# Kernel optimization log

Hardware: AMD Instinct MI355X
Metric: run time of the kernel (lower is better)

## Reference

```python
import jax, jax.numpy as jnp
import numpy as np
from jax import lax

# pywt 'db6' rec_lo (scaling filter). dec_lo = rec_lo[::-1]; pytorch_wavelets
# stores dec filters flipped for conv (=correlation), so analysis correlation
# filters are exactly rec_lo and rec_hi = qmf(rec_lo). Synthesis filters for
# conv_transpose are rec_lo/rec_hi unflipped -> same arrays.
_DB6 = np.array([0.11154074335008017, 0.4946238903983854, 0.7511339080215775,
                 0.3152503517092432, -0.22626469396516913, -0.12976686756709563,
                 0.09750160558707936, 0.02752286553001629, -0.031582039318031156,
                 0.0005538422009938016, 0.004777257511010651, -0.00107730108499558],
                dtype=np.float32)
_QMF = (_DB6[::-1].copy() * ((-1.0) ** np.arange(12))).astype(np.float32)
H0, H1 = jnp.asarray(_DB6), jnp.asarray(_QMF)
LF, J = 12, 3
BATCH, SEQ_LEN, CH = 128, 720, 321
COMP_L = [99, 365, 188, 99]   # [yl, yh1, yh2, yh3] for seq_len=720
OUT_L = [22, 57, 34, 22]      # same decomposition of red_len=104


def afb1d(x):
    """One-level analysis filter bank, mode='symmetric'. x: [B,C,N]."""
    B, C, N = x.shape
    out = (N + LF - 1) // 2                      # pywt dwt_coeff_len (symmetric)
    p = 2 * (out - 1) - N + LF
    xp = jnp.pad(x, ((0, 0), (0, 0), (p // 2, (p + 1) // 2)), mode='symmetric')
    w = jnp.stack([H0, H1])[:, None, :]          # [2,1,LF]
    y = lax.conv_general_dilated(xp.reshape(B * C, 1, -1), w, (2,), 'VALID',
                                 dimension_numbers=('NCH', 'OIH', 'NCH'))
    y = y.reshape(B, C, 2, out)
    return y[:, :, 0], y[:, :, 1]


def sfb1d(lo, hi):
    """One-level synthesis bank == conv_transpose1d(stride=2, padding=LF-2)."""
    B, C, Lin = lo.shape
    z = jnp.stack([lo, hi], axis=2).reshape(B * C, 2, Lin)
    w = jnp.stack([H0[::-1], H1[::-1]])[None]    # [1,2,LF], flipped for corr
    y = lax.conv_general_dilated(z, w, (1,), ((1, 1),), lhs_dilation=(2,),
                                 dimension_numbers=('NCH', 'OIH', 'NCH'))
    return y.reshape(B, C, -1)                   # length 2*Lin + 2 - LF


def sinusoidal_pe(n_pos, d):
    pos = jnp.arange(n_pos, dtype=jnp.float32)[:, None]
    div = jnp.exp(jnp.arange(0, d, 2, dtype=jnp.float32) * (-np.log(10000.0) / d))
    pe = jnp.zeros((n_pos, d), jnp.float32)
    pe = pe.at[:, 0::2].set(jnp.sin(pos * div))
    pe = pe.at[:, 1::2].set(jnp.cos(pos * div[: d // 2]))
    return pe


def _forward(x, qws, qbs, kws, kbs, pws, pbs, iws, als, bes):
    mean = lax.stop_gradient(jnp.mean(x, axis=1, keepdims=True))
    std = lax.stop_gradient(jnp.sqrt(jnp.var(x, axis=1, keepdims=True) + 1e-5))
    xc = jnp.transpose((x - mean) / std, (0, 2, 1))      # [B,C,L]
    yl, yh = xc, []
    for _ in range(J):
        yl, hi = afb1d(yl)
        yh.append(hi)
    decomps = [yl] + yh                                  # lengths COMP_L
    preds = []
    for i, comp in enumerate(decomps):
        B, C, L = comp.shape
        Q = jnp.tanh(comp @ qws[i].T + qbs[i])           # [B,C,L]
        K = jnp.tanh(comp @ kws[i].T + kbs[i])
        scores = jnp.einsum('bcl,bcs->bls', Q, K) / (L ** 0.5)
        weighted = jnp.mean(jnp.tanh(scores), axis=1)    # [B,S] (equal per channel)
        cum = jnp.flip(jnp.cumsum(jnp.flip(weighted, -1), -1), -1)
        P = jax.nn.softmax(cum * als[i][0], axis=-1)
        idxs = jnp.arange(L, dtype=jnp.float32)
        win = jnp.sum(P * idxs, axis=-1)[:, None, None]  # soft truncation [B,1,1]
        mask = jax.nn.sigmoid((idxs[None, None, :] - win) * bes[i][0])
        pred = (comp * mask) @ pws[i].T + pbs[i]         # [B,C,O]
        pred = jax.nn.softmax(iws[i], axis=1) * (pred + sinusoidal_pe(C, pred.shape[-1])[None])
        preds.append(pred)
    ll = preds[0]
    for h in preds[:0:-1]:                               # coarsest high band first
        if ll.shape[-1] > h.shape[-1]:
            ll = ll[..., : h.shape[-1]]
        ll = sfb1d(ll, h)
    return ll, mean, std


def setup_inputs() -> dict:
    key = jax.random.key(0)
    ks = jax.random.split(key, 64)
    inp = {'x': jax.random.normal(ks[0], (BATCH, SEQ_LEN, CH), jnp.float32)}
    k = 1
    for i, (L, O) in enumerate(zip(COMP_L, OUT_L)):
        s = 1.0 / np.sqrt(L)                             # torch Linear default init
        inp[f'qw{i}'] = jax.random.uniform(ks[k], (L, L), jnp.float32, -s, s); k += 1
        inp[f'qb{i}'] = jax.random.uniform(ks[k], (L,), jnp.float32, -s, s); k += 1
        inp[f'kw{i}'] = jax.random.uniform(ks[k], (L, L), jnp.float32, -s, s); k += 1
        inp[f'kb{i}'] = jax.random.uniform(ks[k], (L,), jnp.float32, -s, s); k += 1
        inp[f'pw{i}'] = jnp.full((O, L), 1.0 / L, jnp.float32)
        inp[f'pb{i}'] = jnp.zeros((O,), jnp.float32)
        inp[f'iw{i}'] = jnp.ones((1, CH, O), jnp.float32)
        inp[f'al{i}'] = jnp.full((1,), 10.0, jnp.float32)
        inp[f'be{i}'] = jnp.full((1,), 10.0, jnp.float32)
    return inp


def reference(x, qw0, qb0, kw0, kb0, pw0, pb0, iw0, al0, be0,
              qw1, qb1, kw1, kb1, pw1, pb1, iw1, al1, be1,
              qw2, qb2, kw2, kb2, pw2, pb2, iw2, al2, be2,
              qw3, qb3, kw3, kb3, pw3, pb3, iw3, al3, be3):
    return _forward(x, [qw0, qw1, qw2, qw3], [qb0, qb1, qb2, qb3],
                    [kw0, kw1, kw2, kw3], [kb0, kb1, kb2, kb3],
                    [pw0, pw1, pw2, pw3], [pb0, pb1, pb2, pb3],
                    [iw0, iw1, iw2, iw3], [al0, al1, al2, al3],
                    [be0, be1, be2, be3])
```

## Files before the change

kernel.cpp:

```cpp
#include <hip/hip_runtime.h>
#include <hip/hip_bf16.h>
#include <math.h>

namespace {
constexpr int kB  = 128;
constexpr int kC  = 321;
constexpr int kN0 = 720;
constexpr int kCp = 384;
}

typedef __attribute__((ext_vector_type(8))) short short8;
typedef __attribute__((ext_vector_type(4))) float floatx4;

__constant__ float c_h0[12] = {
  0.11154074335008017f, 0.4946238903983854f, 0.7511339080215775f,
  0.3152503517092432f, -0.22626469396516913f, -0.12976686756709563f,
  0.09750160558707936f, 0.02752286553001629f, -0.031582039318031156f,
  0.0005538422009938016f, 0.004777257511010651f, -0.00107730108499558f};
__constant__ float c_h1[12] = {
  -0.00107730108499558f, -0.004777257511010651f, 0.0005538422009938016f,
  0.031582039318031156f, 0.02752286553001629f, -0.09750160558707936f,
  -0.12976686756709563f, 0.22626469396516913f, 0.3152503517092432f,
  -0.7511339080215775f, 0.4946238903983854f, -0.11154074335008017f};
__constant__ float c_h0r[12] = {
  -0.00107730108499558f, 0.004777257511010651f, 0.0005538422009938016f,
  -0.031582039318031156f, 0.02752286553001629f, 0.09750160558707936f,
  -0.12976686756709563f, -0.22626469396516913f, 0.3152503517092432f,
  0.7511339080215775f, 0.4946238903983854f, 0.11154074335008017f};
__constant__ float c_h1r[12] = {
  -0.11154074335008017f, 0.4946238903983854f, -0.7511339080215775f,
  0.3152503517092432f, 0.22626469396516913f, -0.12976686756709563f,
  -0.09750160558707936f, 0.02752286553001629f, 0.031582039318031156f,
  0.0005538422009938016f, -0.004777257511010651f, -0.00107730108499558f};

__device__ __forceinline__ float fast_tanh(float x) {
  float e = __expf(2.f * x);
  return 1.f - 2.f / (e + 1.f);
}
__device__ __forceinline__ unsigned short f2b(float f) {
  __hip_bfloat16 h = __float2bfloat16(f);
  return __builtin_bit_cast(unsigned short, h);
}

__device__ __forceinline__ void gload16(const unsigned short* g, short* l) {
  __builtin_amdgcn_global_load_lds(
      (const __attribute__((address_space(1))) unsigned int*)g,
      (__attribute__((address_space(3))) unsigned int*)l, 16, 0, 0);
}

__global__ void __launch_bounds__(128) partial_ms_kernel(
    const float* __restrict__ x, float* __restrict__ ps, float* __restrict__ ps2) {
  int b = blockIdx.x, chunk = blockIdx.y;
  int c = blockIdx.z * 128 + threadIdx.x;
  if (c >= kC) return;
  const float* xb = x + (size_t)b * kN0 * kC + c;
  int t0 = chunk * 90;
  float s = 0.f, s2 = 0.f;
#pragma unroll 15
  for (int i = 0; i < 90; ++i) {
    float v = xb[(size_t)(t0 + i) * kC];
    s += v; s2 += v * v;
  }
  ps [(b * 8 + chunk) * kC + c] = s;
  ps2[(b * 8 + chunk) * kC + c] = s2;
}

__global__ void __launch_bounds__(256) finalize_ms_kernel(
    const float* __restrict__ ps, const float* __restrict__ ps2,
    float* __restrict__ mout, float* __restrict__ sout,
    float* __restrict__ meanw, float* __restrict__ invw) {
  int i = blockIdx.x * 256 + threadIdx.x;
  if (i >= kB * kC) return;
  int b = i / kC, c = i - b * kC;
  float s = 0.f, s2 = 0.f;
#pragma unroll
  for (int k = 0; k < 8; ++k) { s += ps[(b * 8 + k) * kC + c]; s2 += ps2[(b * 8 + k) * kC + c]; }
  float mean = s * (1.f / (float)kN0);
  float var = s2 * (1.f / (float)kN0) - mean * mean;
  float sd = sqrtf(var + 1e-5f);
  mout[i] = mean; sout[i] = sd;
  meanw[i] = mean; invw[i] = 1.f / sd;
}

__device__ __forceinline__ int sym_reflect(int t, int N) {
  t = (t < 0) ? (-1 - t) : t;
  t = (t >= N) ? (2 * N - 1 - t) : t;
  return t;
}

template <bool NORM, bool LO_F32, bool LO_BF16>
__global__ void __launch_bounds__(256) dwt_fused_kernel(
    const float* __restrict__ in, const float* __restrict__ meanw,
    const float* __restrict__ invw, float* __restrict__ loF,
    unsigned short* __restrict__ loB, unsigned short* __restrict__ hiB,
    int N, int L, int Lp) {
  __shared__ float xs[138][64];
  __shared__ unsigned short los[64][72];
  __shared__ unsigned short his[64][72];
  const int b = blockIdx.z;
  const int n0 = blockIdx.x * 64, c0 = blockIdx.y * 64;
  const int tid = threadIdx.x;
  const int cl = tid & 63, wv = tid >> 6;
  const int c = c0 + cl;
  const int t0 = 2 * n0 - 10;
  const float* ib = in + (size_t)b * N * kC;
  float mean = 0.f, inv = 1.f;
  if (NORM && c < kC) { mean = meanw[b * kC + c]; inv = invw[b * kC + c]; }
  for (int r = wv; r < 138; r += 4) {
    int t = sym_reflect(t0 + r, N);
    float v = (c < kC) ? ib[(size_t)t * kC + c] : 0.f;
    if (NORM) v = (v - mean) * inv;
    xs[r][cl] = v;
  }
  __syncthreads();
#pragma unroll 4
  for (int k = 0; k < 16; ++k) {
    int nl = wv + 4 * k;
    int n = n0 + nl;
    float a0 = 0.f, a1 = 0.f;
    int base = 2 * nl;
#pragma unroll
    for (int j = 0; j < 12; ++j) {
      float v = xs[base + j][cl];
      a0 += v * c_h0[j]; a1 += v * c_h1[j];
    }
    bool valid = (n < L) && (c < kC);
    if (LO_F32 && valid) loF[((size_t)b * L + n) * kC + c] = a0;
    if (LO_BF16) los[cl][nl] = f2b(valid ? a0 : 0.f);
    his[cl][nl] = f2b(valid ? a1 : 0.f);
  }
  __syncthreads();
  int row = tid >> 2, part = tid & 3;
  size_t dst = ((size_t)b * kCp + c0 + row) * Lp + n0 + part * 16;
  *(uint4*)(hiB + dst)     = *(const uint4*)&his[row][part * 16];
  *(uint4*)(hiB + dst + 8) = *(const uint4*)&his[row][part * 16 + 8];
  if (LO_BF16) {
    *(uint4*)(loB + dst)     = *(const uint4*)&los[row][part * 16];
    *(uint4*)(loB + dst + 8) = *(const uint4*)&los[row][part * 16 + 8];
  }
}

struct WcArgs { const float* src[8]; unsigned short* dst[8]; int L[8]; int Lp[8]; };
__global__ void __launch_bounds__(256) wconv_all_kernel(WcArgs a) {
  int lvl = blockIdx.y;
  int Lp = a.Lp[lvl], L = a.L[lvl];
  int i = blockIdx.x * 256 + threadIdx.x;
  if (i >= Lp * Lp) return;
  int p = i / Lp, l = i - p * Lp;
  a.dst[lvl][i] = f2b((p < L && l < L) ? a.src[lvl][(size_t)p * L + l] : 0.f);
}

struct QKAllArgs {
  const unsigned short* W[8];
  const unsigned short* Xt[4];
  const float* bias[8];
  unsigned short* Y[8];
  int Lp[4], L[4], yOff[4];
};
__global__ void __launch_bounds__(512, 4) qk_all_kernel(QKAllArgs a) {
  const int y = blockIdx.y;
  const int lvl = (y >= a.yOff[1]) + (y >= a.yOff[2]) + (y >= a.yOff[3]);
  const int Lp = a.Lp[lvl], L = a.L[lvl];
  const int pBase = (y - a.yOff[lvl]) * 128;
  const unsigned short* W0 = a.W[2 * lvl]     + (size_t)pBase * Lp;
  const unsigned short* W1 = a.W[2 * lvl + 1] + (size_t)pBase * Lp;
  const int b = blockIdx.z;
  const int cBase = blockIdx.x * 64;
  const int tid = threadIdx.x;
  const int ln = tid & 63, w = tid >> 6;
  __shared__ short smem[2 * 320 * 64];
  floatx4 acc[2][4] = {};
  const unsigned short* Xb = a.Xt[lvl] + ((size_t)b * kCp + cBase) * Lp;
  const int lrow = ln >> 3;
  const int gswz = ((ln & 7) ^ lrow) << 3;
  const unsigned short* srcs[5];
#pragma unroll
  for (int i = 0; i < 5; ++i) {
    int o = w * 5 + i;
    int rr = o * 8 + lrow;
    const unsigned short* s = (o < 16) ? (W0 + (size_t)rr * Lp)
                            : (o < 32) ? (W1 + (size_t)(rr - 128) * Lp)
                                       : (Xb + (size_t)(rr - 256) * Lp);
    srcs[i] = s + gswz;
  }
  const int nt = Lp >> 6;
#pragma unroll
  for (int i = 0; i < 5; ++i) gload16(srcs[i], &smem[(w * 5 + i) * 512]);
  __syncthreads();
  for (int kt = 0; kt < nt; ++kt) {
    const int ph = (kt & 1) * 20480;
    if (kt + 1 < nt) {
      const int phn = ((kt + 1) & 1) * 20480;
      const int lc = (kt + 1) << 6;
#pragma unroll
      for (int i = 0; i < 5; ++i) gload16(srcs[i] + lc, &smem[phn + (w * 5 + i) * 512]);
    }
#pragma unroll
    for (int sub = 0; sub < 2; ++sub) {
      const int sc = (((ln >> 4) + sub * 4) ^ (ln & 7)) << 3;
      const int ar = (w * 16 + (ln & 15)) * 64 + sc;
      short8 aq = *(const short8*)&smem[ph + ar];
      short8 ak = *(const short8*)&smem[ph + 8192 + ar];
      short8 bv[4];
#pragma unroll
      for (int ni = 0; ni < 4; ++ni)
        bv[ni] = *(const short8*)&smem[ph + 16384 + (ni * 16 + (ln & 15)) * 64 + sc];
#pragma unroll
      for (int ni = 0; ni < 4; ++ni) {
        acc[0][ni] = __builtin_amdgcn_mfma_f32_16x16x32_bf16(aq, bv[ni], acc[0][ni], 0, 0, 0);
        acc[1][ni] = __builtin_amdgcn_mfma_f32_16x16x32_bf16(ak, bv[ni], acc[1][ni], 0, 0, 0);
      }
    }
    __syncthreads();
  }
#pragma unroll
  for (int s = 0; s < 2; ++s) {
    const float* bias = a.bias[2 * lvl + s];
    unsigned short* Yd = a.Y[2 * lvl + s];
#pragma unroll
    for (int r = 0; r < 4; ++r) {
      int p = pBase + w * 16 + (ln >> 4) * 4 + r;
      bool pv = (p < L);
      float bvf = pv ? bias[p] : 0.f;
#pragma unroll
      for (int ni = 0; ni < 4; ++ni) {
        int c = cBase + ni * 16 + (ln & 15);
        float v = fast_tanh(acc[s][ni][r] + bvf);
        if (s == 0) { if (!pv) v = 0.f; }
        else        { if (c >= kC) v = 0.f; }
        Yd[((size_t)b * Lp + p) * kCp + c] = f2b(v);
      }
    }
  }
}

struct ScAllArgs {
  const unsigned short* Q[4]; const unsigned short* K[4];
  float* wgt[4];
  int Lp[4], L[4], tOff[4];
  float scale[4];
};
__global__ void __launch_bounds__(512, 4) scores_all_kernel(ScAllArgs a) {
  const int t = blockIdx.x;
  const int lvl = (t >= a.tOff[1]) + (t >= a.tOff[2]) + (t >= a.tOff[3]);
  const int rel = t - a.tOff[lvl];
  const int Lp = a.Lp[lvl], L = a.L[lvl];
  const int pt = Lp >> 7;
  const int sBase = (rel % pt) * 128;
  const int lBase = (rel / pt) * 128;
  const int b = blockIdx.y;
  const int tid = threadIdx.x;
  const int ln = tid & 63, w = tid >> 6;
  const int wm = w & 3, wn = w >> 2;
  __shared__ short smem[2 * 256 * 64];
  __shared__ float red[128];
  floatx4 acc[2][4] = {};
  const unsigned short* Qp = a.Q[lvl] + ((size_t)b * Lp + lBase) * kCp;
  const unsigned short* Kp = a.K[lvl] + ((size_t)b * Lp + sBase) * kCp;
  const int lrow = ln >> 3;
  const int gswz = ((ln & 7) ^ lrow) << 3;
  const unsigned short* srcs[4];
#pragma unroll
  for (int i = 0; i < 4; ++i) {
    int o = w * 4 + i;
    int rr = o * 8 + lrow;
    srcs[i] = ((o < 16) ? (Qp + (size_t)rr * kCp)
                        : (Kp + (size_t)(rr - 128) * kCp)) + gswz;
  }
#pragma unroll
  for (int i = 0; i < 4; ++i) gload16(srcs[i], &smem[(w * 4 + i) * 512]);
  if (tid < 128) red[tid] = 0.f;
  __syncthreads();
  const int nt = kCp >> 6;
  for (int kt = 0; kt < nt; ++kt) {
    const int ph = (kt & 1) * 16384;
    if (kt + 1 < nt) {
      const int phn = ((kt + 1) & 1) * 16384;
      const int cc = (kt + 1) << 6;
#pragma unroll
      for (int i = 0; i < 4; ++i) gload16(srcs[i] + cc, &smem[phn + (w * 4 + i) * 512]);
    }
#pragma unroll
    for (int sub = 0; sub < 2; ++sub) {
      const int sc = (((ln >> 4) + sub * 4) ^ (ln & 7)) << 3;
      short8 av[2], bv[4];
#pragma unroll
      for (int mi = 0; mi < 2; ++mi)
        av[mi] = *(const short8*)&smem[ph + (wm * 32 + mi * 16 + (ln & 15)) * 64 + sc];
#pragma unroll
      for (int ni = 0; ni < 4; ++ni)
        bv[ni] = *(const short8*)&smem[ph + 8192 + (wn * 64 + ni * 16 + (ln & 15)) * 64 + sc];
#pragma unroll
      for (int mi = 0; mi < 2; ++mi)
#pragma unroll
        for (int ni = 0; ni < 4; ++ni)
          acc[mi][ni] = __builtin_amdgcn_mfma_f32_16x16x32_bf16(av[mi], bv[ni], acc[mi][ni], 0, 0, 0);
    }
    __syncthreads();
  }
  const float scale = a.scale[lvl];
#pragma unroll
  for (int ni = 0; ni < 4; ++ni) {
    float p = 0.f;
#pragma unroll
    for (int mi = 0; mi < 2; ++mi)
#pragma unroll
      for (int r = 0; r < 4; ++r) p += fast_tanh(acc[mi][ni][r] * scale);
    p += __shfl_xor(p, 16);
    p += __shfl_xor(p, 32);
    if ((ln & 48) == 0) atomicAdd(&red[wn * 64 + ni * 16 + (ln & 15)], p);
  }
  __syncthreads();
  if (tid < 128) {
    int s = sBase + tid;
    if (s < L) atomicAdd(&a.wgt[lvl][(size_t)b * L + s], red[tid]);
  }
}

struct WinArgs { const float* wgt[4]; const float* al[4]; const float* be[4];
                 float* mask[4]; int L[4]; };
__global__ void __launch_bounds__(64) winmask_all_kernel(WinArgs a) {
  int lvl = blockIdx.y;
  int b = blockIdx.x, lane = threadIdx.x;
  int L = a.L[lvl];
  const float* wgt = a.wgt[lvl] + (size_t)b * L;
  float al = a.al[lvl][0], be = a.be[lvl][0];
  float invL = 1.f / (float)L;
  int chunk = (L + 63) >> 6;
  int s0 = lane * chunk;
  float v[6];
  float csum = 0.f;
  for (int i = chunk - 1; i >= 0; --i) {
    int s = s0 + i;
    float xv = (s < L) ? wgt[s] * invL : 0.f;
    csum += xv; v[i] = csum;
  }
  float tot = csum;
  for (int o = 1; o < 64; o <<= 1) {
    float t = __shfl_down(tot, o);
    if (lane + o < 64) tot += t;
  }
  float excl = tot - csum;
  float m = -1e30f;
  for (int i = 0; i < chunk; ++i)
    if (s0 + i < L) m = fmaxf(m, al * (v[i] + excl));
  for (int o = 32; o; o >>= 1) m = fmaxf(m, __shfl_xor(m, o));
  float sum = 0.f, num = 0.f;
  for (int i = 0; i < chunk; ++i) {
    int s = s0 + i;
    if (s < L) { float e = __expf(al * (v[i] + excl) - m); sum += e; num += e * (float)s; }
  }
  for (int o = 32; o; o >>= 1) { sum += __shfl_xor(sum, o); num += __shfl_xor(num, o); }
  float win = num / sum;
  float* mk = a.mask[lvl] + (size_t)b * L;
  for (int i = 0; i < chunk; ++i) {
    int s = s0 + i;
    if (s < L) mk[s] = 1.f / (1.f + __expf(-((float)s - win) * be));
  }
}

struct IwArgs { const float* iw[4]; float* sm[4]; int O[4]; };
__global__ void __launch_bounds__(64) iwsm_all_kernel(IwArgs a) {
  int x = blockIdx.x;
  int lvl, o;
  if (x < 22) { lvl = 0; o = x; }
  else if (x < 79) { lvl = 1; o = x - 22; }
  else if (x < 113) { lvl = 2; o = x - 79; }
  else { lvl = 3; o = x - 113; }
  int O = a.O[lvl];
  const float* iw = a.iw[lvl];
  int lane = threadIdx.x;
  float m = -1e30f;
  for (int c = lane; c < kC; c += 64) m = fmaxf(m, iw[c * O + o]);
  for (int k = 32; k; k >>= 1) m = fmaxf(m, __shfl_xor(m, k));
  float sum = 0.f;
  for (int c = lane; c < kC; c += 64) sum += __expf(iw[c * O + o] - m);
  for (int k = 32; k; k >>= 1) sum += __shfl_xor(sum, k);
  float inv = 1.f / sum;
  for (int c = lane; c < kC; c += 64) a.sm[lvl][c * O + o] = __expf(iw[c * O + o] - m) * inv;
}

struct PredAllArgs {
  const unsigned short* Xt[4];
  const float* PW[4]; const float* PB[4]; const float* MK[4]; const float* SM[4];
  float* OUT[4];
  int L[4], Lp[4], O[4];
};
__global__ void __launch_bounds__(256) pred_all_kernel(PredAllArgs a) {
  const int lvl = blockIdx.y;
  const int L = a.L[lvl], Lp = a.Lp[lvl], O = a.O[lvl];
  const float* PW = a.PW[lvl];
  const int b = blockIdx.z;
  const int cBase = blockIdx.x * 128;
  const int tid = threadIdx.x;
  const int ln = tid & 63, w = tid >> 6;
  __shared__ short As[64 * 40];
  __shared__ short Bs[128 * 40];
  floatx4 acc[8] = {};
  const unsigned short* Xb = a.Xt[lvl] + ((size_t)b * kCp + cBase) * Lp;
  const float* mk = a.MK[lvl] + (size_t)b * L;
  for (int lc = 0; lc < Lp; lc += 32) {
    {
      int o = tid >> 2, j0 = (tid & 3) * 8;
      alignas(16) unsigned short tmp[8];
#pragma unroll
      for (int j = 0; j < 8; ++j) {
        int l = lc + j0 + j;
        float v = (o < O && l < L) ? PW[(size_t)o * L + l] * mk[l] : 0.f;
        tmp[j] = f2b(v);
      }
      *(uint4*)&As[o * 40 + j0] = *(const uint4*)tmp;
    }
#pragma unroll
    for (int q = 0; q < 2; ++q) {
      int ch = tid * 2 + q;
      int row = ch >> 2, pos = ch & 3;
      *(uint4*)(&Bs[row * 40 + pos * 8]) = *(const uint4*)(Xb + (size_t)row * Lp + lc + pos * 8);
    }
    __syncthreads();
    short8 av = *(const short8*)&As[(w * 16 + (ln & 15)) * 40 + (ln >> 4) * 8];
#pragma unroll
    for (int ni = 0; ni < 8; ++ni) {
      short8 bb = *(const short8*)&Bs[(ni * 16 + (ln & 15)) * 40 + (ln >> 4) * 8];
      acc[ni] = __builtin_amdgcn_mfma_f32_16x16x32_bf16(av, bb, acc[ni], 0, 0, 0);
    }
    __syncthreads();
  }
  const float negln = -logf(10000.f) / (float)O;
#pragma unroll
  for (int ni = 0; ni < 8; ++ni) {
    int c = cBase + ni * 16 + (ln & 15);
    if (c >= kC) continue;
#pragma unroll
    for (int r = 0; r < 4; ++r) {
      int o = w * 16 + (ln >> 4) * 4 + r;
      if (o >= O) continue;
      float dv = __expf(negln * (float)(2 * (o >> 1)));
      float ang = (float)c * dv;
      float pe = (o & 1) ? cosf(ang) : sinf(ang);
      a.OUT[lvl][((size_t)b * O + o) * kC + c] = a.SM[lvl][c * O + o] * (acc[ni][r] + a.PB[lvl][o] + pe);
    }
  }
}

__global__ void __launch_bounds__(256) sfb_fused_kernel(
    const float* __restrict__ P0, const float* __restrict__ P1,
    const float* __restrict__ P2, const float* __restrict__ P3,
    float* __restrict__ out) {
  __shared__ float p0s[22][32], p3s[22][32], p2s[34][32], p1s[57][32];
  __shared__ float r1s[34][32], r2s[58][32];
  __shared__ float outs[104][33];
  int b = blockIdx.y, c0 = blockIdx.x * 32;
  int tid = threadIdx.x;
  int cl = tid & 31, r = tid >> 5;
  int c = c0 + cl;
  bool cv = c < kC;
  for (int o = r; o < 22; o += 8) {
    p0s[o][cl] = cv ? P0[((size_t)b * 22 + o) * kC + c] : 0.f;
    p3s[o][cl] = cv ? P3[((size_t)b * 22 + o) * kC + c] : 0.f;
  }
  for (int o = r; o < 34; o += 8) p2s[o][cl] = cv ? P2[((size_t)b * 34 + o) * kC + c] : 0.f;
  for (int o = r; o < 57; o += 8) p1s[o][cl] = cv ? P1[((size_t)b * 57 + o) * kC + c] : 0.f;
  __syncthreads();
  for (int n = r; n < 34; n += 8) {
    float acc = 0.f;
#pragma unroll
    for (int j = 0; j < 12; ++j) {
      int m = n + j - 1;
      if (m < 0 || (m & 1)) continue;
      int i = m >> 1;
      if (i >= 22) continue;
      acc += c_h0r[j] * p0s[i][cl] + c_h1r[j] * p3s[i][cl];
    }
    r1s[n][cl] = acc;
  }
  __syncthreads();
  for (int n = r; n < 58; n += 8) {
    float acc = 0.f;
#pragma unroll
    for (int j = 0; j < 12; ++j) {
      int m = n + j - 1;
      if (m < 0 || (m & 1)) continue;
      int i = m >> 1;
      if (i >= 34) continue;
      acc += c_h0r[j] * r1s[i][cl] + c_h1r[j] * p2s[i][cl];
    }
    r2s[n][cl] = acc;
  }
  __syncthreads();
  for (int n = r; n < 104; n += 8) {
    float acc = 0.f;
#pragma unroll
    for (int j = 0; j < 12; ++j) {
      int m = n + j - 1;
      if (m < 0 || (m & 1)) continue;
      int i = m >> 1;
      if (i >= 57) continue;
      acc += c_h0r[j] * r2s[i][cl] + c_h1r[j] * p1s[i][cl];
    }
    outs[n][cl] = acc;
  }
  __syncthreads();
  for (int idx = tid; idx < 32 * 104; idx += 256) {
    int ci = idx / 104, n = idx - ci * 104;
    int cg = c0 + ci;
    if (cg < kC) out[((size_t)b * kC + cg) * 104 + n] = outs[n][ci];
  }
}

extern "C" void kernel_launch(void* const* d_in, const int* in_sizes, int n_in,
                              void* d_out, int out_size, void* d_ws, size_t ws_size,
                              hipStream_t stream) {
  (void)in_sizes; (void)n_in; (void)out_size; (void)ws_size;
  const float* x = (const float*)d_in[0];
  auto inp = [&](int lvl, int j) { return (const float*)d_in[1 + 9 * lvl + j]; };

  float* outf = (float*)d_out;
  float* mout = outf + (size_t)kB * kC * 104;
  float* sout = mout + (size_t)kB * kC;

  float* Wp = (float*)d_ws;
  size_t off = 0;
  auto alloc = [&](size_t n) { float* p = Wp + off; off += (n + 63) & ~(size_t)63; return p; };

  float* LO1 = alloc((size_t)kB * 365 * kC);
  float* LO2 = alloc((size_t)kB * 188 * kC);
  unsigned short* Xt1 = (unsigned short*)alloc((size_t)kB * kCp * 384 / 2);
  unsigned short* Xt2 = (unsigned short*)alloc((size_t)kB * kCp * 256 / 2);
  unsigned short* Xt0 = (unsigned short*)alloc((size_t)kB * kCp * 128 / 2);
  unsigned short* Xt3 = (unsigned short*)alloc((size_t)kB * kCp * 128 / 2);
  unsigned short* KbfAll = (unsigned short*)alloc((size_t)kB * kCp * 896 / 2);
  unsigned short* Wpv[8];
  for (int i = 0; i < 8; ++i)
    Wpv[i] = (unsigned short*)alloc((size_t)384 * 384 / 2);
  float* wgtAll = alloc((size_t)kB * (99 + 365 + 188 + 99));
  float* M0 = alloc((size_t)kB * 99);  float* M1 = alloc((size_t)kB * 365);
  float* M2 = alloc((size_t)kB * 188); float* M3 = alloc((size_t)kB * 99);
  float* S0 = alloc((size_t)kC * 22);  float* S1 = alloc((size_t)kC * 57);
  float* S2 = alloc((size_t)kC * 34);  float* S3 = alloc((size_t)kC * 22);
  float* P0 = alloc((size_t)kB * 22 * kC); float* P1 = alloc((size_t)kB * 57 * kC);
  float* P2 = alloc((size_t)kB * 34 * kC); float* P3 = alloc((size_t)kB * 22 * kC);
  float* ps   = alloc((size_t)kB * 8 * kC);
  float* ps2  = alloc((size_t)kB * 8 * kC);
  float* meanw = alloc((size_t)kB * kC);
  float* invw  = alloc((size_t)kB * kC);
  unsigned short* QbfAll = (unsigned short*)LO1;

  const int Lc[4]  = {99, 365, 188, 99};
  const int Lpv[4] = {128, 384, 256, 128};
  const int Ov[4]  = {22, 57, 34, 22};
  const int prefLp[4] = {0, 128, 512, 768};
  const int wOff[4] = {0, 99, 99 + 365, 99 + 365 + 188};
  unsigned short* Qlvl[4]; unsigned short* Klvl[4];
  for (int i = 0; i < 4; ++i) {
    Qlvl[i] = QbfAll + (size_t)kB * kCp * prefLp[i];
    Klvl[i] = KbfAll + (size_t)kB * kCp * prefLp[i];
  }
  const unsigned short* Xts[4] = {Xt0, Xt1, Xt2, Xt3};
  float* masks[4] = {M0, M1, M2, M3};
  float* smws[4]  = {S0, S1, S2, S3};
  float* preds[4] = {P0, P1, P2, P3};

  partial_ms_kernel<<<dim3(kB, 8, 3), 128, 0, stream>>>(x, ps, ps2);
  finalize_ms_kernel<<<(kB * kC + 255) / 256, 256, 0, stream>>>(ps, ps2, mout, sout, meanw, invw);

  dwt_fused_kernel<true, true, false><<<dim3(6, kCp / 64, kB), 256, 0, stream>>>(
      x, meanw, invw, LO1, nullptr, Xt1, kN0, 365, 384);
  dwt_fused_kernel<false, true, false><<<dim3(4, kCp / 64, kB), 256, 0, stream>>>(
      LO1, nullptr, nullptr, LO2, nullptr, Xt2, 365, 188, 256);
  dwt_fused_kernel<false, false, true><<<dim3(2, kCp / 64, kB), 256, 0, stream>>>(
      LO2, nullptr, nullptr, nullptr, Xt0, Xt3, 188, 99, 128);

  {
    WcArgs wa;
    for (int i = 0; i < 4; ++i) {
      wa.src[2 * i] = inp(i, 0); wa.src[2 * i + 1] = inp(i, 2);
      wa.dst[2 * i] = Wpv[2 * i]; wa.dst[2 * i + 1] = Wpv[2 * i + 1];
      wa.L[2 * i] = wa.L[2 * i + 1] = Lc[i];
      wa.Lp[2 * i] = wa.Lp[2 * i + 1] = Lpv[i];
    }
    wconv_all_kernel<<<dim3(576, 8), 256, 0, stream>>>(wa);
  }
  hipMemsetAsync(wgtAll, 0, (size_t)kB * (99 + 365 + 188 + 99) * sizeof(float), stream);

  {
    QKAllArgs qa;
    for (int i = 0; i < 4; ++i) {
      qa.W[2 * i] = Wpv[2 * i]; qa.W[2 * i + 1] = Wpv[2 * i + 1];
      qa.bias[2 * i] = inp(i, 1); qa.bias[2 * i + 1] = inp(i, 3);
      qa.Y[2 * i] = Qlvl[i]; qa.Y[2 * i + 1] = Klvl[i];
      qa.Xt[i] = Xts[i]; qa.Lp[i] = Lpv[i]; qa.L[i] = Lc[i];
    }
    qa.yOff[0] = 0; qa.yOff[1] = 1; qa.yOff[2] = 4; qa.yOff[3] = 6;
    qk_all_kernel<<<dim3(kCp / 64, 7, kB), 512, 0, stream>>>(qa);
  }

  {
    ScAllArgs sa;
    for (int i = 0; i < 4; ++i) {
      sa.Q[i] = Qlvl[i]; sa.K[i] = Klvl[i];
      sa.wgt[i] = wgtAll + (size_t)kB * wOff[i];
      sa.Lp[i] = Lpv[i]; sa.L[i] = Lc[i];
      sa.scale[i] = 1.0f / sqrtf((float)Lc[i]);
    }
    sa.tOff[0] = 0; sa.tOff[1] = 1; sa.tOff[2] = 10; sa.tOff[3] = 14;
    scores_all_kernel<<<dim3(15, kB), 512, 0, stream>>>(sa);
  }

  {
    WinArgs wa;
    for (int i = 0; i < 4; ++i) {
      wa.wgt[i] = wgtAll + (size_t)kB * wOff[i];
      wa.al[i] = inp(i, 7); wa.be[i] = inp(i, 8);
      wa.mask[i] = masks[i]; wa.L[i] = Lc[i];
    }
    winmask_all_kernel<<<dim3(kB, 4), 64, 0, stream>>>(wa);
    IwArgs ia;
    for (int i = 0; i < 4; ++i) { ia.iw[i] = inp(i, 6); ia.sm[i] = smws[i]; ia.O[i] = Ov[i]; }
    iwsm_all_kernel<<<135, 64, 0, stream>>>(ia);
  }

  {
    PredAllArgs pa;
    for (int i = 0; i < 4; ++i) {
      pa.Xt[i] = Xts[i]; pa.PW[i] = inp(i, 4); pa.PB[i] = inp(i, 5);
      pa.MK[i] = masks[i]; pa.SM[i] = smws[i]; pa.OUT[i] = preds[i];
      pa.L[i] = Lc[i]; pa.Lp[i] = Lpv[i]; pa.O[i] = Ov[i];
    }
    pred_all_kernel<<<dim3(kCp / 128, 4, kB), 256, 0, stream>>>(pa);
  }

  sfb_fused_kernel<<<dim3(11, kB), 256, 0, stream>>>(P0, P1, P2, P3, outf);
}
```

Before: 808.2 us.

## Halve K-tile in QK and score GEMMs and merge window/softmax kernels

The QK projection and score GEMM kernels now use a 32-wide K tile instead of 64. This halves their shared memory, and their launch bounds are raised to allow 8 blocks per SM, aiming for higher occupancy and better latency hiding. The XOR swizzle on shared-memory loads is dropped, which may bring bank conflicts, and twice as many loop iterations with barriers are needed. The window-mask and input-weight softmax kernels are merged into one launch to save a kernel launch.

```diff
diff --git a/kernel.cpp b/kernel.cpp
--- a/kernel.cpp
+++ b/kernel.cpp
@@ -157,7 +157,7 @@
   unsigned short* Y[8];
   int Lp[4], L[4], yOff[4];
 };
-__global__ void __launch_bounds__(512, 4) qk_all_kernel(QKAllArgs a) {
+__global__ void __launch_bounds__(512, 8) qk_all_kernel(QKAllArgs a) {
   const int y = blockIdx.y;
   const int lvl = (y >= a.yOff[1]) + (y >= a.yOff[2]) + (y >= a.yOff[3]);
   const int Lp = a.Lp[lvl], L = a.L[lvl];
@@ -168,48 +168,49 @@
   const int cBase = blockIdx.x * 64;
   const int tid = threadIdx.x;
   const int ln = tid & 63, w = tid >> 6;
-  __shared__ short smem[2 * 320 * 64];
+  __shared__ short smem[2 * 320 * 32];
   floatx4 acc[2][4] = {};
   const unsigned short* Xb = a.Xt[lvl] + ((size_t)b * kCp + cBase) * Lp;
-  const int lrow = ln >> 3;
-  const int gswz = ((ln & 7) ^ lrow) << 3;
-  const unsigned short* srcs[5];
-#pragma unroll
-  for (int i = 0; i < 5; ++i) {
-    int o = w * 5 + i;
-    int rr = o * 8 + lrow;
-    const unsigned short* s = (o < 16) ? (W0 + (size_t)rr * Lp)
-                            : (o < 32) ? (W1 + (size_t)(rr - 128) * Lp)
+  const int lr = ln >> 2;
+  const int ck = (ln & 3) * 8;
+  const int nld = (w < 4) ? 3 : 2;
+  const int ow0 = (w < 4) ? w * 3 : 12 + (w - 4) * 2;
+  const unsigned short* srcs[3];
+#pragma unroll
+  for (int i = 0; i < 3; ++i) {
+    int o = (i < nld) ? (ow0 + i) : ow0;
+    int rr = o * 16 + lr;
+    const unsigned short* s = (o < 8)  ? (W0 + (size_t)rr * Lp)
+                            : (o < 16) ? (W1 + (size_t)(rr - 128) * Lp)
                                        : (Xb + (size_t)(rr - 256) * Lp);
-    srcs[i] = s + gswz;
-  }
-  const int nt = Lp >> 6;
-#pragma unroll
-  for (int i = 0; i < 5; ++i) gload16(srcs[i], &smem[(w * 5 + i) * 512]);
+    srcs[i] = s + ck;
+  }
+  const int nt = Lp >> 5;
+#pragma unroll
+  for (int i = 0; i < 3; ++i)
+    if (i < nld) gload16(srcs[i], &smem[(ow0 + i) * 512]);
   __syncthreads();
   for (int kt = 0; kt < nt; ++kt) {
-    const int ph = (kt & 1) * 20480;
     if (kt + 1 < nt) {
-      const int phn = ((kt + 1) & 1) * 20480;
-      const int lc = (kt + 1) << 6;
-#pragma unroll
-      for (int i = 0; i < 5; ++i) gload16(srcs[i] + lc, &smem[phn + (w * 5 + i) * 512]);
-    }
-#pragma unroll
-    for (int sub = 0; sub < 2; ++sub) {
-      const int sc = (((ln >> 4) + sub * 4) ^ (ln & 7)) << 3;
-      const int ar = (w * 16 + (ln & 15)) * 64 + sc;
-      short8 aq = *(const short8*)&smem[ph + ar];
-      short8 ak = *(const short8*)&smem[ph + 8192 + ar];
-      short8 bv[4];
-#pragma unroll
-      for (int ni = 0; ni < 4; ++ni)
-        bv[ni] = *(const short8*)&smem[ph + 16384 + (ni * 16 + (ln & 15)) * 64 + sc];
-#pragma unroll
-      for (int ni = 0; ni < 4; ++ni) {
-        acc[0][ni] = __builtin_amdgcn_mfma_f32_16x16x32_bf16(aq, bv[ni], acc[0][ni], 0, 0, 0);
-        acc[1][ni] = __builtin_amdgcn_mfma_f32_16x16x32_bf16(ak, bv[ni], acc[1][ni], 0, 0, 0);
-      }
+      const int phn = ((kt + 1) & 1) * 10240;
+      const int lc = (kt + 1) << 5;
+#pragma unroll
+      for (int i = 0; i < 3; ++i)
+        if (i < nld) gload16(srcs[i] + lc, &smem[phn + (ow0 + i) * 512]);
+    }
+    const int ph = (kt & 1) * 10240;
+    const int ko = (ln >> 4) * 8;
+    const int ar = (w * 16 + (ln & 15)) * 32 + ko;
+    short8 aq = *(const short8*)&smem[ph + ar];
+    short8 ak = *(const short8*)&smem[ph + 4096 + ar];
+    short8 bv[4];
+#pragma unroll
+    for (int ni = 0; ni < 4; ++ni)
+      bv[ni] = *(const short8*)&smem[ph + 8192 + (ni * 16 + (ln & 15)) * 32 + ko];
+#pragma unroll
+    for (int ni = 0; ni < 4; ++ni) {
+      acc[0][ni] = __builtin_amdgcn_mfma_f32_16x16x32_bf16(aq, bv[ni], acc[0][ni], 0, 0, 0);
+      acc[1][ni] = __builtin_amdgcn_mfma_f32_16x16x32_bf16(ak, bv[ni], acc[1][ni], 0, 0, 0);
     }
     __syncthreads();
   }
@@ -240,7 +241,7 @@
   int Lp[4], L[4], tOff[4];
   float scale[4];
 };
-__global__ void __launch_bounds__(512, 4) scores_all_kernel(ScAllArgs a) {
+__global__ void __launch_bounds__(512, 8) scores_all_kernel(ScAllArgs a) {
   const int t = blockIdx.x;
   const int lvl = (t >= a.tOff[1]) + (t >= a.tOff[2]) + (t >= a.tOff[3]);
   const int rel = t - a.tOff[lvl];
@@ -252,50 +253,47 @@
   const int tid = threadIdx.x;
   const int ln = tid & 63, w = tid >> 6;
   const int wm = w & 3, wn = w >> 2;
-  __shared__ short smem[2 * 256 * 64];
+  __shared__ short smem[2 * 256 * 32];
   __shared__ float red[128];
   floatx4 acc[2][4] = {};
   const unsigned short* Qp = a.Q[lvl] + ((size_t)b * Lp + lBase) * kCp;
   const unsigned short* Kp = a.K[lvl] + ((size_t)b * Lp + sBase) * kCp;
-  const int lrow = ln >> 3;
-  const int gswz = ((ln & 7) ^ lrow) << 3;
-  const unsigned short* srcs[4];
-#pragma unroll
-  for (int i = 0; i < 4; ++i) {
-    int o = w * 4 + i;
-    int rr = o * 8 + lrow;
-    srcs[i] = ((o < 16) ? (Qp + (size_t)rr * kCp)
-                        : (Kp + (size_t)(rr - 128) * kCp)) + gswz;
-  }
-#pragma unroll
-  for (int i = 0; i < 4; ++i) gload16(srcs[i], &smem[(w * 4 + i) * 512]);
+  const int lr = ln >> 2;
+  const int ck = (ln & 3) * 8;
+  const unsigned short* srcs[2];
+#pragma unroll
+  for (int i = 0; i < 2; ++i) {
+    int o = w * 2 + i;
+    int rr = o * 16 + lr;
+    srcs[i] = ((o < 8) ? (Qp + (size_t)rr * kCp)
+                       : (Kp + (size_t)(rr - 128) * kCp)) + ck;
+  }
+#pragma unroll
+  for (int i = 0; i < 2; ++i) gload16(srcs[i], &smem[(w * 2 + i) * 512]);
   if (tid < 128) red[tid] = 0.f;
   __syncthreads();
-  const int nt = kCp >> 6;
+  const int nt = kCp >> 5;
   for (int kt = 0; kt < nt; ++kt) {
-    const int ph = (kt & 1) * 16384;
     if (kt + 1 < nt) {
-      const int phn = ((kt + 1) & 1) * 16384;
-      const int cc = (kt + 1) << 6;
-#pragma unroll
-      for (int i = 0; i < 4; ++i) gload16(srcs[i] + cc, &smem[phn + (w * 4 + i) * 512]);
-    }
-#pragma unroll
-    for (int sub = 0; sub < 2; ++sub) {
-      const int sc = (((ln >> 4) + sub * 4) ^ (ln & 7)) << 3;
-      short8 av[2], bv[4];
-#pragma unroll
-      for (int mi = 0; mi < 2; ++mi)
-        av[mi] = *(const short8*)&smem[ph + (wm * 32 + mi * 16 + (ln & 15)) * 64 + sc];
+      const int phn = ((kt + 1) & 1) * 8192;
+      const int cc = (kt + 1) << 5;
+#pragma unroll
+      for (int i = 0; i < 2; ++i) gload16(srcs[i] + cc, &smem[phn + (w * 2 + i) * 512]);
+    }
+    const int ph = (kt & 1) * 8192;
+    const int ko = (ln >> 4) * 8;
+    short8 av[2], bv[4];
+#pragma unroll
+    for (int mi = 0; mi < 2; ++mi)
+      av[mi] = *(const short8*)&smem[ph + (wm * 32 + mi * 16 + (ln & 15)) * 32 + ko];
+#pragma unroll
+    for (int ni = 0; ni < 4; ++ni)
+      bv[ni] = *(const short8*)&smem[ph + 4096 + (wn * 64 + ni * 16 + (ln & 15)) * 32 + ko];
+#pragma unroll
+    for (int mi = 0; mi < 2; ++mi)
 #pragma unroll
       for (int ni = 0; ni < 4; ++ni)
-        bv[ni] = *(const short8*)&smem[ph + 8192 + (wn * 64 + ni * 16 + (ln & 15)) * 64 + sc];
-#pragma unroll
-      for (int mi = 0; mi < 2; ++mi)
-#pragma unroll
-        for (int ni = 0; ni < 4; ++ni)
-          acc[mi][ni] = __builtin_amdgcn_mfma_f32_16x16x32_bf16(av[mi], bv[ni], acc[mi][ni], 0, 0, 0);
-    }
+        acc[mi][ni] = __builtin_amdgcn_mfma_f32_16x16x32_bf16(av[mi], bv[ni], acc[mi][ni], 0, 0, 0);
     __syncthreads();
   }
   const float scale = a.scale[lvl];
@@ -317,67 +315,69 @@
   }
 }
 
-struct WinArgs { const float* wgt[4]; const float* al[4]; const float* be[4];
-                 float* mask[4]; int L[4]; };
-__global__ void __launch_bounds__(64) winmask_all_kernel(WinArgs a) {
-  int lvl = blockIdx.y;
-  int b = blockIdx.x, lane = threadIdx.x;
-  int L = a.L[lvl];
-  const float* wgt = a.wgt[lvl] + (size_t)b * L;
-  float al = a.al[lvl][0], be = a.be[lvl][0];
-  float invL = 1.f / (float)L;
-  int chunk = (L + 63) >> 6;
-  int s0 = lane * chunk;
-  float v[6];
-  float csum = 0.f;
-  for (int i = chunk - 1; i >= 0; --i) {
-    int s = s0 + i;
-    float xv = (s < L) ? wgt[s] * invL : 0.f;
-    csum += xv; v[i] = csum;
-  }
-  float tot = csum;
-  for (int o = 1; o < 64; o <<= 1) {
-    float t = __shfl_down(tot, o);
-    if (lane + o < 64) tot += t;
-  }
-  float excl = tot - csum;
-  float m = -1e30f;
-  for (int i = 0; i < chunk; ++i)
-    if (s0 + i < L) m = fmaxf(m, al * (v[i] + excl));
-  for (int o = 32; o; o >>= 1) m = fmaxf(m, __shfl_xor(m, o));
-  float sum = 0.f, num = 0.f;
-  for (int i = 0; i < chunk; ++i) {
-    int s = s0 + i;
-    if (s < L) { float e = __expf(al * (v[i] + excl) - m); sum += e; num += e * (float)s; }
-  }
-  for (int o = 32; o; o >>= 1) { sum += __shfl_xor(sum, o); num += __shfl_xor(num, o); }
-  float win = num / sum;
-  float* mk = a.mask[lvl] + (size_t)b * L;
-  for (int i = 0; i < chunk; ++i) {
-    int s = s0 + i;
-    if (s < L) mk[s] = 1.f / (1.f + __expf(-((float)s - win) * be));
-  }
-}
-
-struct IwArgs { const float* iw[4]; float* sm[4]; int O[4]; };
-__global__ void __launch_bounds__(64) iwsm_all_kernel(IwArgs a) {
-  int x = blockIdx.x;
-  int lvl, o;
-  if (x < 22) { lvl = 0; o = x; }
-  else if (x < 79) { lvl = 1; o = x - 22; }
-  else if (x < 113) { lvl = 2; o = x - 79; }
-  else { lvl = 3; o = x - 113; }
-  int O = a.O[lvl];
-  const float* iw = a.iw[lvl];
+struct WinIwArgs {
+  const float* wgt[4]; const float* al[4]; const float* be[4];
+  float* mask[4]; int L[4];
+  const float* iw[4]; float* sm[4]; int O[4];
+};
+__global__ void __launch_bounds__(64) winiw_kernel(WinIwArgs a) {
+  int bx = blockIdx.x;
   int lane = threadIdx.x;
-  float m = -1e30f;
-  for (int c = lane; c < kC; c += 64) m = fmaxf(m, iw[c * O + o]);
-  for (int k = 32; k; k >>= 1) m = fmaxf(m, __shfl_xor(m, k));
-  float sum = 0.f;
-  for (int c = lane; c < kC; c += 64) sum += __expf(iw[c * O + o] - m);
-  for (int k = 32; k; k >>= 1) sum += __shfl_xor(sum, k);
-  float inv = 1.f / sum;
-  for (int c = lane; c < kC; c += 64) a.sm[lvl][c * O + o] = __expf(iw[c * O + o] - m) * inv;
+  if (bx < 512) {
+    int lvl = bx >> 7, b = bx & 127;
+    int L = a.L[lvl];
+    const float* wgt = a.wgt[lvl] + (size_t)b * L;
+    float al = a.al[lvl][0], be = a.be[lvl][0];
+    float invL = 1.f / (float)L;
+    int chunk = (L + 63) >> 6;
+    int s0 = lane * chunk;
+    float v[6];
+    float csum = 0.f;
+    for (int i = chunk - 1; i >= 0; --i) {
+      int s = s0 + i;
+      float xv = (s < L) ? wgt[s] * invL : 0.f;
+      csum += xv; v[i] = csum;
+    }
+    float tot = csum;
+    for (int o = 1; o < 64; o <<= 1) {
+      float t = __shfl_down(tot, o);
+      if (lane + o < 64) tot += t;
+    }
+    float excl = tot - csum;
+    float m = -1e30f;
+    for (int i = 0; i < chunk; ++i)
+      if (s0 + i < L) m = fmaxf(m, al * (v[i] + excl));
+    for (int o = 32; o; o >>= 1) m = fmaxf(m, __shfl_xor(m, o));
+    float sum = 0.f, num = 0.f;
+    for (int i = 0; i < chunk; ++i) {
+      int s = s0 + i;
+      if (s < L) { float e = __expf(al * (v[i] + excl) - m); sum += e; num += e * (float)s; }
+    }
+    for (int o = 32; o; o >>= 1) { sum += __shfl_xor(sum, o); num += __shfl_xor(num, o); }
+    float win = num / sum;
+    float* mk = a.mask[lvl] + (size_t)b * L;
+    for (int i = 0; i < chunk; ++i) {
+      int s = s0 + i;
+      if (s < L) mk[s] = 1.f / (1.f + __expf(-((float)s - win) * be));
+    }
+  } else {
+    int x = bx - 512;
+    int lvl, o;
+    if (x < 22) { lvl = 0; o = x; }
+    else if (x < 79) { lvl = 1; o = x - 22; }
+    else if (x < 113) { lvl = 2; o = x - 79; }
+    else { lvl = 3; o = x - 113; }
+    int O = a.O[lvl];
+    const float* iw = a.iw[lvl];
+    float m = -1e30f;
+    for (int c = lane; c < kC; c += 64) m = fmaxf(m, iw[c * O + o]);
+    for (int k = 32; k; k >>= 1) m = fmaxf(m, __shfl_xor(m, k));
+    float sum = 0.f;
+    for (int c = lane; c < kC; c += 64) sum += __expf(iw[c * O + o] - m);
+    for (int k = 32; k; k >>= 1) sum += __shfl_xor(sum, k);
+    float inv = 1.f / sum;
+    for (int c = lane; c < kC; c += 64) a.sm[lvl][c * O + o] = __expf(iw[c * O + o] - m) * inv;
+  }
 }
 
 struct PredAllArgs {
@@ -608,16 +608,14 @@
   }
 
   {
-    WinArgs wa;
+    WinIwArgs wa;
     for (int i = 0; i < 4; ++i) {
       wa.wgt[i] = wgtAll + (size_t)kB * wOff[i];
       wa.al[i] = inp(i, 7); wa.be[i] = inp(i, 8);
       wa.mask[i] = masks[i]; wa.L[i] = Lc[i];
-    }
-    winmask_all_kernel<<<dim3(kB, 4), 64, 0, stream>>>(wa);
-    IwArgs ia;
-    for (int i = 0; i < 4; ++i) { ia.iw[i] = inp(i, 6); ia.sm[i] = smws[i]; ia.O[i] = Ov[i]; }
-    iwsm_all_kernel<<<135, 64, 0, stream>>>(ia);
+      wa.iw[i] = inp(i, 6); wa.sm[i] = smws[i]; wa.O[i] = Ov[i];
+    }
+    winiw_kernel<<<512 + 135, 64, 0, stream>>>(wa);
   }
 
   {
```

Measured after the change: 795.0 us. About the same (-1.6%).
